# Optimization experiments

Measured on AMD Instinct MI355X. Metric: run time of the kernel, lower is better.

Reference implementation:

```python
import jax, jax.numpy as jnp
import numpy as np
from jax import lax

B, RES, C, HEADS = 32, 56, 256, 8
HSP, WSP = RES, 7            # idx == 0: horizontal stripes
HD = C // HEADS
S = HSP * WSP                # tokens per window
SCALE = HD ** -0.5


def setup_inputs() -> dict:
    key = jax.random.key(0)
    kq, kk, kv, kw, kb = jax.random.split(key, 5)
    N = RES * RES
    return {
        "q": jax.random.normal(kq, (B, N, C), jnp.float32),
        "k": jax.random.normal(kk, (B, N, C), jnp.float32),
        "v": jax.random.normal(kv, (B, N, C), jnp.float32),
        "w_conv": jax.random.normal(kw, (3, 3, 1, C), jnp.float32) * 0.05,  # HWIO depthwise
        "b_conv": jax.random.normal(kb, (C,), jnp.float32) * 0.05,
    }


def _to_windows(x):
    # [B, N, C] -> [B*nW, HSP, WSP, C], window grid (RES//HSP, RES//WSP)
    x = x.reshape(B, RES // HSP, HSP, RES // WSP, WSP, C)
    x = x.transpose(0, 1, 3, 2, 4, 5)
    return x.reshape(-1, HSP, WSP, C)


def _to_heads(xw):
    # [B*nW, HSP, WSP, C] -> [B*nW, heads, S, hd]
    return xw.reshape(-1, S, HEADS, HD).transpose(0, 2, 1, 3)


def reference(q, k, v, w_conv, b_conv):
    qw = _to_heads(_to_windows(q)) * SCALE          # [BW, h, S, hd]
    kw = _to_heads(_to_windows(k))
    vw_img = _to_windows(v)                          # [BW, HSP, WSP, C]
    # LePE: depthwise 3x3 conv on each window image
    lepe = lax.conv_general_dilated(
        vw_img, w_conv, (1, 1), "SAME",
        dimension_numbers=("NHWC", "HWIO", "NHWC"),
        feature_group_count=C,
    ) + b_conv
    vw = _to_heads(vw_img)
    lepe = _to_heads(lepe)
    attn = jnp.einsum("bhqd,bhkd->bhqk", qw, kw)    # [BW, h, S, S]
    attn = jax.nn.softmax(attn, axis=-1)
    out = jnp.einsum("bhqk,bhkd->bhqd", attn, vw) + lepe
    # merge heads and windows back to [B, N, C]
    out = out.transpose(0, 2, 1, 3).reshape(B, RES // HSP, RES // WSP, HSP, WSP, C)
    out = out.transpose(0, 1, 3, 2, 4, 5).reshape(B, RES * RES, C)
    return out
```

## Files before the change

### kernel.cpp

```cpp
#include <hip/hip_runtime.h>
#include <stdint.h>

typedef __attribute__((ext_vector_type(8))) short short8;
typedef __attribute__((ext_vector_type(4))) short s16x4;
typedef __attribute__((ext_vector_type(4))) float f32x4;
typedef __attribute__((ext_vector_type(2))) float f32x2;
typedef __attribute__((ext_vector_type(4))) uint32_t uint32x4;

#define RES 56
#define NCH 256
#define SW 392
#define SP 416

#define KP_OFF   0
#define VT_OFF   25600
#define WB_OFF   52224
#define BB_OFF   53376
#define SC_OFF   53504
#define SMEM_SZ  62720

__device__ __forceinline__ uint32_t cvtpk(float lo, float hi) {
    uint32_t r;
    asm("v_cvt_pk_bf16_f32 %0, %1, %2" : "=v"(r) : "v"(lo), "v"(hi));
    return r;
}
__device__ __forceinline__ float bf2f(short s) {
    return __uint_as_float(((uint32_t)(uint16_t)s) << 16);
}

__global__ __launch_bounds__(256, 2) void lepe_attn_kernel(
    const float* __restrict__ qg, const float* __restrict__ kg,
    const float* __restrict__ vg, const float* __restrict__ wg,
    const float* __restrict__ bg, float* __restrict__ outg)
{
    __shared__ __align__(16) char smem[SMEM_SZ];
    short* kpan = (short*)(smem + KP_OFF);
    short* vtb  = (short*)(smem + VT_OFF);
    float* wbuf = (float*)(smem + WB_OFF);
    float* bbuf = (float*)(smem + BB_OFF);

    const int tid  = threadIdx.x;
    const int lane = tid & 63;
    const int wv   = tid >> 6;
    const int col  = lane & 15;
    const int g    = lane >> 4;

    const int h  = blockIdx.x & 7;
    const int bw = blockIdx.x >> 3;
    const int s  = bw & 7;
    const int b  = bw >> 3;

    const int cb = h * 32;
    const int tb = b * (RES * RES);

    for (int i = tid; i < 288; i += 256)
        wbuf[i] = wg[(i >> 5) * NCH + cb + (i & 31)];
    if (tid < 32)
        bbuf[tid] = bg[cb + tid];

    #pragma unroll
    for (int p0 = 0; p0 < 1792; p0 += 256) {
        int idx = p0 + tid;
        if (idx < 1664) {
            int tok = idx >> 2;
            int hd8 = (idx & 3) << 3;
            f32x4 ka = {0.f,0.f,0.f,0.f}, kb2 = ka, va = ka, vb = ka;
            if (tok < SW) {
                int y  = (tok * 9363) >> 16;
                int xx = tok - y * 7;
                int n  = y * RES + s * 7 + xx;
                int off = (tb + n) * NCH + cb + hd8;
                ka  = *(const f32x4*)(kg + off);
                kb2 = *(const f32x4*)(kg + off + 4);
                va  = *(const f32x4*)(vg + off);
                vb  = *(const f32x4*)(vg + off + 4);
            }
            if (tok < 400) {
                uint32x4 kv;
                kv[0] = cvtpk(ka[0],  ka[1]);
                kv[1] = cvtpk(ka[2],  ka[3]);
                kv[2] = cvtpk(kb2[0], kb2[1]);
                kv[3] = cvtpk(kb2[2], kb2[3]);
                *(uint32x4*)(kpan + (hd8 >> 3) * 3200 + tok * 8) = kv;
            }
            uint32_t v01 = cvtpk(va[0], va[1]);
            uint32_t v23 = cvtpk(va[2], va[3]);
            uint32_t v45 = cvtpk(vb[0], vb[1]);
            uint32_t v67 = cvtpk(vb[2], vb[3]);
            int swl = (hd8 & 12) << 1;
            int ta  = tok ^ swl;
            int tc  = tok ^ (swl + 8);
            short* vr = vtb + hd8 * SP;
            vr[ta] = (short)v01;         vr += SP;
            vr[ta] = (short)(v01 >> 16); vr += SP;
            vr[ta] = (short)v23;         vr += SP;
            vr[ta] = (short)(v23 >> 16); vr += SP;
            vr[tc] = (short)v45;         vr += SP;
            vr[tc] = (short)(v45 >> 16); vr += SP;
            vr[tc] = (short)v67;         vr += SP;
            vr[tc] = (short)(v67 >> 16);
        }
    }
    __syncthreads();

    const float SCL = 0.17677669529663688f * 1.4426950408889634f;
    const f32x4 zero4 = {0.f, 0.f, 0.f, 0.f};
    const float NINF = -__builtin_inff();
    const short* kg0 = kpan + g * 3200 + col * 8;

    for (int qt = wv; qt < 25; qt += 4) {
        int qrow = (qt << 4) + col;
        int tq = qrow < SW ? qrow : SW - 1;
        int yq = (tq * 9363) >> 16;
        int nq = yq * RES + s * 7 + (tq - yq * 7);
        short8 qf;
        {
            int qoff = (tb + nq) * NCH + cb + (g << 3);
            f32x4 qa = *(const f32x4*)(qg + qoff);
            f32x4 qb = *(const f32x4*)(qg + qoff + 4);
            union { uint32_t u[4]; short8 s8; } qu;
            qu.u[0] = cvtpk(qa[0]*SCL, qa[1]*SCL);
            qu.u[1] = cvtpk(qa[2]*SCL, qa[3]*SCL);
            qu.u[2] = cvtpk(qb[0]*SCL, qb[1]*SCL);
            qu.u[3] = cvtpk(qb[2]*SCL, qb[3]*SCL);
            qf = qu.s8;
        }

        f32x4 Sf[25];
        #pragma unroll
        for (int kt = 0; kt < 25; ++kt) {
            short8 kf = *(const short8*)(kg0 + kt * 128);
            Sf[kt] = __builtin_amdgcn_mfma_f32_16x16x32_bf16(kf, qf, zero4, 0, 0, 0);
        }
        #pragma unroll
        for (int r = 0; r < 4; ++r) Sf[24][r] = (g >= 2) ? NINF : Sf[24][r];

        float m = NINF;
        #pragma unroll
        for (int kt = 0; kt < 25; ++kt) {
            #pragma unroll
            for (int r = 0; r < 4; ++r) m = fmaxf(m, Sf[kt][r]);
        }
        m = fmaxf(m, __shfl_xor(m, 16));
        m = fmaxf(m, __shfl_xor(m, 32));

        uint32_t pk[25][2];
        float l = 0.f;
        #pragma unroll
        for (int kt = 0; kt < 25; ++kt) {
            float p0 = exp2f(Sf[kt][0] - m);
            float p1 = exp2f(Sf[kt][1] - m);
            float p2 = exp2f(Sf[kt][2] - m);
            float p3 = exp2f(Sf[kt][3] - m);
            uint32_t u01 = __builtin_amdgcn_perm(__float_as_uint(p1), __float_as_uint(p0), 0x07060302u);
            uint32_t u23 = __builtin_amdgcn_perm(__float_as_uint(p3), __float_as_uint(p2), 0x07060302u);
            pk[kt][0] = u01; pk[kt][1] = u23;
            l += __uint_as_float(u01 << 16) + __uint_as_float(u01 & 0xffff0000u)
               + __uint_as_float(u23 << 16) + __uint_as_float(u23 & 0xffff0000u);
        }
        l += __shfl_xor(l, 16);
        l += __shfl_xor(l, 32);
        float invl = 1.0f / l;

        f32x4 O0a = zero4, O0b = zero4, O1a = zero4, O1b = zero4;
        const short* vl = vtb + col * SP;
        const short* vh = vl + 16 * SP;
        const int vsw = (col & 12) << 1;
        const int gof = g << 2;
        #pragma unroll
        for (int kt = 0; kt < 25; ++kt) {
            int tokx = ((kt << 4) + gof) ^ vsw;
            s16x4 a0 = *(const s16x4*)(vl + tokx);
            s16x4 a1 = *(const s16x4*)(vh + tokx);
            union { uint32_t u[2]; s16x4 s4; } pu;
            pu.u[0] = pk[kt][0]; pu.u[1] = pk[kt][1];
            if (kt & 1) {
                O0b = __builtin_amdgcn_mfma_f32_16x16x16bf16_1k(a0, pu.s4, O0b, 0, 0, 0);
                O1b = __builtin_amdgcn_mfma_f32_16x16x16bf16_1k(a1, pu.s4, O1b, 0, 0, 0);
            } else {
                O0a = __builtin_amdgcn_mfma_f32_16x16x16bf16_1k(a0, pu.s4, O0a, 0, 0, 0);
                O1a = __builtin_amdgcn_mfma_f32_16x16x16bf16_1k(a1, pu.s4, O1a, 0, 0, 0);
            }
        }

        float* scr = (float*)(smem + SC_OFF + wv * 2304);
        {
            int d = lane >> 1, half = lane & 1;
            int t0 = (qt << 4) + (half << 3);
            int dsw = (d & 12) << 1;
            const short* vrow = vtb + d * SP;
            float vals[24];
            #pragma unroll
            for (int kk = 0; kk < 3; ++kk) {
                int t8 = t0 - 8 + (kk << 3);
                if (t8 < 0) t8 = 0;
                short8 bv = *(const short8*)(vrow + (t8 ^ dsw));
                #pragma unroll
                for (int j = 0; j < 8; ++j) vals[kk * 8 + j] = bf2f(bv[j]);
            }
            float wr[9];
            #pragma unroll
            for (int t9 = 0; t9 < 9; ++t9) wr[t9] = wbuf[t9 * 32 + d];
            float bs = bbuf[d];
            float o[8];
            #pragma unroll
            for (int i = 0; i < 8; ++i) {
                int t = t0 + i;
                int yy = (t * 9363) >> 16;
                int xxi = t - yy * 7;
                float mlft = (xxi == 0) ? 0.f : 1.f;
                float mrgt = (xxi == 6) ? 0.f : 1.f;
                float mu   = (t >= 7)   ? 1.f : 0.f;
                float md   = (t <= 384) ? 1.f : 0.f;
                float top = wr[0]*(vals[i]*mlft)    + wr[1]*vals[i+1]  + wr[2]*(vals[i+2]*mrgt);
                float mid = wr[3]*(vals[i+7]*mlft)  + wr[4]*vals[i+8]  + wr[5]*(vals[i+9]*mrgt);
                float bot = wr[6]*(vals[i+14]*mlft) + wr[7]*vals[i+15] + wr[8]*(vals[i+16]*mrgt);
                o[i] = bs + mid + mu * top + md * bot;
            }
            #pragma unroll
            for (int mm = 0; mm < 4; ++mm) {
                f32x2 pr = {o[2*mm], o[2*mm+1]};
                *(f32x2*)(scr + d * 18 + (half << 3) + 2 * mm) = pr;
            }
        }

        f32x4 r0, r1;
        #pragma unroll
        for (int r = 0; r < 4; ++r) {
            r0[r] = (O0a[r] + O0b[r]) * invl + scr[(4 * g + r) * 18 + col];
            r1[r] = (O1a[r] + O1b[r]) * invl + scr[(16 + 4 * g + r) * 18 + col];
        }
        if (qrow < SW) {
            float* op = outg + (tb + nq) * NCH + cb + (g << 2);
            *(f32x4*)op = r0;
            *(f32x4*)(op + 16) = r1;
        }
    }
}

extern "C" void kernel_launch(void* const* d_in, const int* in_sizes, int n_in,
                              void* d_out, int out_size, void* d_ws, size_t ws_size,
                              hipStream_t stream) {
    const float* q  = (const float*)d_in[0];
    const float* k  = (const float*)d_in[1];
    const float* v  = (const float*)d_in[2];
    const float* wc = (const float*)d_in[3];
    const float* bc = (const float*)d_in[4];
    float* out = (float*)d_out;
    hipLaunchKernelGGL(lepe_attn_kernel, dim3(2048), dim3(256), 0, stream,
                       q, k, v, wc, bc, out);
}
```

Measured before the change: 409.1 us.

## Pad V-transpose with zero halo, move row sums to MFMA, use max3

Result: slower. 419.2 us (+2.5%).

```diff
diff --git a/kernel.cpp b/kernel.cpp
--- a/kernel.cpp
+++ b/kernel.cpp
@@ -10,14 +10,15 @@
 #define RES 56
 #define NCH 256
 #define SW 392
-#define SP 416
+#define SP 424
+#define TSH 8
 
 #define KP_OFF   0
 #define VT_OFF   25600
-#define WB_OFF   52224
-#define BB_OFF   53376
-#define SC_OFF   53504
-#define SMEM_SZ  62720
+#define WB_OFF   52736
+#define BB_OFF   53888
+#define SC_OFF   54016
+#define SMEM_SZ  63232
 
 __device__ __forceinline__ uint32_t cvtpk(float lo, float hi) {
     uint32_t r;
@@ -26,6 +27,11 @@
 }
 __device__ __forceinline__ float bf2f(short s) {
     return __uint_as_float(((uint32_t)(uint16_t)s) << 16);
+}
+__device__ __forceinline__ float max3f(float a, float b, float c) {
+    float r;
+    asm("v_max3_f32 %0, %1, %2, %3" : "=v"(r) : "v"(a), "v"(b), "v"(c));
+    return r;
 }
 
 __global__ __launch_bounds__(256, 2) void lepe_attn_kernel(
@@ -58,47 +64,47 @@
     if (tid < 32)
         bbuf[tid] = bg[cb + tid];
 
-    #pragma unroll
-    for (int p0 = 0; p0 < 1792; p0 += 256) {
-        int idx = p0 + tid;
-        if (idx < 1664) {
-            int tok = idx >> 2;
-            int hd8 = (idx & 3) << 3;
-            f32x4 ka = {0.f,0.f,0.f,0.f}, kb2 = ka, va = ka, vb = ka;
-            if (tok < SW) {
-                int y  = (tok * 9363) >> 16;
-                int xx = tok - y * 7;
-                int n  = y * RES + s * 7 + xx;
-                int off = (tb + n) * NCH + cb + hd8;
-                ka  = *(const f32x4*)(kg + off);
-                kb2 = *(const f32x4*)(kg + off + 4);
-                va  = *(const f32x4*)(vg + off);
-                vb  = *(const f32x4*)(vg + off + 4);
-            }
-            if (tok < 400) {
-                uint32x4 kv;
-                kv[0] = cvtpk(ka[0],  ka[1]);
-                kv[1] = cvtpk(ka[2],  ka[3]);
-                kv[2] = cvtpk(kb2[0], kb2[1]);
-                kv[3] = cvtpk(kb2[2], kb2[3]);
-                *(uint32x4*)(kpan + (hd8 >> 3) * 3200 + tok * 8) = kv;
-            }
-            uint32_t v01 = cvtpk(va[0], va[1]);
-            uint32_t v23 = cvtpk(va[2], va[3]);
-            uint32_t v45 = cvtpk(vb[0], vb[1]);
-            uint32_t v67 = cvtpk(vb[2], vb[3]);
-            int swl = (hd8 & 12) << 1;
-            int ta  = tok ^ swl;
-            int tc  = tok ^ (swl + 8);
-            short* vr = vtb + hd8 * SP;
-            vr[ta] = (short)v01;         vr += SP;
-            vr[ta] = (short)(v01 >> 16); vr += SP;
-            vr[ta] = (short)v23;         vr += SP;
-            vr[ta] = (short)(v23 >> 16); vr += SP;
-            vr[tc] = (short)v45;         vr += SP;
-            vr[tc] = (short)(v45 >> 16); vr += SP;
-            vr[tc] = (short)v67;         vr += SP;
-            vr[tc] = (short)(v67 >> 16);
+    vtb[(tid >> 3) * SP + (tid & 7)] = 0;
+
+    {
+        const int hd8 = wv << 3;
+        #pragma unroll
+        for (int it = 0; it < 7; ++it) {
+            int tok = (it << 6) + lane;
+            if (tok < 416) {
+                f32x4 ka = {0.f,0.f,0.f,0.f}, kb2 = ka, va = ka, vb = ka;
+                if (tok < SW) {
+                    int y  = (tok * 9363) >> 16;
+                    int xx = tok - y * 7;
+                    int n  = y * RES + s * 7 + xx;
+                    int off = (tb + n) * NCH + cb + hd8;
+                    ka  = *(const f32x4*)(kg + off);
+                    kb2 = *(const f32x4*)(kg + off + 4);
+                    va  = *(const f32x4*)(vg + off);
+                    vb  = *(const f32x4*)(vg + off + 4);
+                }
+                if (tok < 400) {
+                    uint32x4 kv;
+                    kv[0] = cvtpk(ka[0],  ka[1]);
+                    kv[1] = cvtpk(ka[2],  ka[3]);
+                    kv[2] = cvtpk(kb2[0], kb2[1]);
+                    kv[3] = cvtpk(kb2[2], kb2[3]);
+                    *(uint32x4*)(kpan + wv * 3200 + tok * 8) = kv;
+                }
+                uint32_t v01 = cvtpk(va[0], va[1]);
+                uint32_t v23 = cvtpk(va[2], va[3]);
+                uint32_t v45 = cvtpk(vb[0], vb[1]);
+                uint32_t v67 = cvtpk(vb[2], vb[3]);
+                short* vr = vtb + hd8 * SP + tok + TSH;
+                vr[0]      = (short)v01;
+                vr[SP]     = (short)(v01 >> 16);
+                vr[2*SP]   = (short)v23;
+                vr[3*SP]   = (short)(v23 >> 16);
+                vr[4*SP]   = (short)v45;
+                vr[5*SP]   = (short)(v45 >> 16);
+                vr[6*SP]   = (short)v67;
+                vr[7*SP]   = (short)(v67 >> 16);
+            }
         }
     }
     __syncthreads();
@@ -107,6 +113,9 @@
     const f32x4 zero4 = {0.f, 0.f, 0.f, 0.f};
     const float NINF = -__builtin_inff();
     const short* kg0 = kpan + g * 3200 + col * 8;
+
+    s16x4 ones;
+    ones[0] = ones[1] = ones[2] = ones[3] = (short)0x3F80;
 
     for (int qt = wv; qt < 25; qt += 4) {
         int qrow = (qt << 4) + col;
@@ -138,42 +147,33 @@
         float m = NINF;
         #pragma unroll
         for (int kt = 0; kt < 25; ++kt) {
-            #pragma unroll
-            for (int r = 0; r < 4; ++r) m = fmaxf(m, Sf[kt][r]);
+            m = max3f(m, Sf[kt][0], Sf[kt][1]);
+            m = max3f(m, Sf[kt][2], Sf[kt][3]);
         }
         m = fmaxf(m, __shfl_xor(m, 16));
         m = fmaxf(m, __shfl_xor(m, 32));
 
         uint32_t pk[25][2];
-        float l = 0.f;
         #pragma unroll
         for (int kt = 0; kt < 25; ++kt) {
             float p0 = exp2f(Sf[kt][0] - m);
             float p1 = exp2f(Sf[kt][1] - m);
             float p2 = exp2f(Sf[kt][2] - m);
             float p3 = exp2f(Sf[kt][3] - m);
-            uint32_t u01 = __builtin_amdgcn_perm(__float_as_uint(p1), __float_as_uint(p0), 0x07060302u);
-            uint32_t u23 = __builtin_amdgcn_perm(__float_as_uint(p3), __float_as_uint(p2), 0x07060302u);
-            pk[kt][0] = u01; pk[kt][1] = u23;
-            l += __uint_as_float(u01 << 16) + __uint_as_float(u01 & 0xffff0000u)
-               + __uint_as_float(u23 << 16) + __uint_as_float(u23 & 0xffff0000u);
-        }
-        l += __shfl_xor(l, 16);
-        l += __shfl_xor(l, 32);
-        float invl = 1.0f / l;
-
-        f32x4 O0a = zero4, O0b = zero4, O1a = zero4, O1b = zero4;
-        const short* vl = vtb + col * SP;
-        const short* vh = vl + 16 * SP;
-        const int vsw = (col & 12) << 1;
-        const int gof = g << 2;
-        #pragma unroll
-        for (int kt = 0; kt < 25; ++kt) {
-            int tokx = ((kt << 4) + gof) ^ vsw;
-            s16x4 a0 = *(const s16x4*)(vl + tokx);
-            s16x4 a1 = *(const s16x4*)(vh + tokx);
+            pk[kt][0] = __builtin_amdgcn_perm(__float_as_uint(p1), __float_as_uint(p0), 0x07060302u);
+            pk[kt][1] = __builtin_amdgcn_perm(__float_as_uint(p3), __float_as_uint(p2), 0x07060302u);
+        }
+
+        f32x4 O0a = zero4, O0b = zero4, O1a = zero4, O1b = zero4, lac = zero4;
+        const short* va0 = vtb + col * SP + TSH + (g << 2);
+        const short* va1 = va0 + 16 * SP;
+        #pragma unroll
+        for (int kt = 0; kt < 25; ++kt) {
+            s16x4 a0 = *(const s16x4*)(va0 + (kt << 4));
+            s16x4 a1 = *(const s16x4*)(va1 + (kt << 4));
             union { uint32_t u[2]; s16x4 s4; } pu;
             pu.u[0] = pk[kt][0]; pu.u[1] = pk[kt][1];
+            lac = __builtin_amdgcn_mfma_f32_16x16x16bf16_1k(ones, pu.s4, lac, 0, 0, 0);
             if (kt & 1) {
                 O0b = __builtin_amdgcn_mfma_f32_16x16x16bf16_1k(a0, pu.s4, O0b, 0, 0, 0);
                 O1b = __builtin_amdgcn_mfma_f32_16x16x16bf16_1k(a1, pu.s4, O1b, 0, 0, 0);
@@ -182,19 +182,17 @@
                 O1a = __builtin_amdgcn_mfma_f32_16x16x16bf16_1k(a1, pu.s4, O1a, 0, 0, 0);
             }
         }
+        float invl = __builtin_amdgcn_rcpf(lac[0]);
 
         float* scr = (float*)(smem + SC_OFF + wv * 2304);
         {
             int d = lane >> 1, half = lane & 1;
             int t0 = (qt << 4) + (half << 3);
-            int dsw = (d & 12) << 1;
             const short* vrow = vtb + d * SP;
             float vals[24];
             #pragma unroll
             for (int kk = 0; kk < 3; ++kk) {
-                int t8 = t0 - 8 + (kk << 3);
-                if (t8 < 0) t8 = 0;
-                short8 bv = *(const short8*)(vrow + (t8 ^ dsw));
+                short8 bv = *(const short8*)(vrow + t0 + (kk << 3));
                 #pragma unroll
                 for (int j = 0; j < 8; ++j) vals[kk * 8 + j] = bf2f(bv[j]);
             }
@@ -210,12 +208,10 @@
                 int xxi = t - yy * 7;
                 float mlft = (xxi == 0) ? 0.f : 1.f;
                 float mrgt = (xxi == 6) ? 0.f : 1.f;
-                float mu   = (t >= 7)   ? 1.f : 0.f;
-                float md   = (t <= 384) ? 1.f : 0.f;
-                float top = wr[0]*(vals[i]*mlft)    + wr[1]*vals[i+1]  + wr[2]*(vals[i+2]*mrgt);
-                float mid = wr[3]*(vals[i+7]*mlft)  + wr[4]*vals[i+8]  + wr[5]*(vals[i+9]*mrgt);
-                float bot = wr[6]*(vals[i+14]*mlft) + wr[7]*vals[i+15] + wr[8]*(vals[i+16]*mrgt);
-                o[i] = bs + mid + mu * top + md * bot;
+                o[i] = bs
+                     + wr[0]*(vals[i]*mlft)    + wr[1]*vals[i+1]  + wr[2]*(vals[i+2]*mrgt)
+                     + wr[3]*(vals[i+7]*mlft)  + wr[4]*vals[i+8]  + wr[5]*(vals[i+9]*mrgt)
+                     + wr[6]*(vals[i+14]*mlft) + wr[7]*vals[i+15] + wr[8]*(vals[i+16]*mrgt);
             }
             #pragma unroll
             for (int mm = 0; mm < 4; ++mm) {
```
